# Kernel tuning notes

Measured on AMD Instinct MI355X. Metric: run time of the kernel, lower is better.

Reference implementation:

```python
import jax, jax.numpy as jnp
import numpy as np

B, T, E, H = 2, 2048, 1024, 16


def setup_inputs() -> dict:
    key = jax.random.key(0)
    ks = jax.random.split(key, 8)
    # VarianceScaling(1.0) ~ truncated normal with stddev ~ sqrt(1/fan_in)
    std = 1.0 / np.sqrt(E)
    x = jax.random.normal(ks[0], (B, T, E), dtype=jnp.float32)
    y = jax.random.normal(ks[1], (B, T, E), dtype=jnp.float32)
    # causal mask [1, 1, T, T]
    mask = jnp.tril(jnp.ones((T, T), dtype=jnp.float32))[None, None]
    Wq = jax.random.normal(ks[2], (E, E), dtype=jnp.float32) * std
    Wk = jax.random.normal(ks[3], (E, E), dtype=jnp.float32) * std
    Wv = jax.random.normal(ks[4], (E, E), dtype=jnp.float32) * std
    Wo = jax.random.normal(ks[5], (E, E), dtype=jnp.float32) * std
    bq = jnp.zeros((E,), jnp.float32)
    bk = jnp.zeros((E,), jnp.float32)
    bv = jnp.zeros((E,), jnp.float32)
    bo = jnp.zeros((E,), jnp.float32)
    return {"x": x, "y": y, "mask": mask, "Wq": Wq, "bq": bq,
            "Wk": Wk, "bk": bk, "Wv": Wv, "bv": bv, "Wo": Wo, "bo": bo,
            "num_heads": H}


def reference(x, y, mask, Wq, bq, Wk, bk, Wv, bv, Wo, bo, num_heads):
    Bx, Tq, Emb = x.shape
    Tkv = y.shape[1]
    d = Emb // num_heads
    q = (x @ Wq + bq).reshape(Bx, Tq, num_heads, d)
    k = (y @ Wk + bk).reshape(Bx, Tkv, num_heads, d)
    v = (y @ Wv + bv).reshape(Bx, Tkv, num_heads, d)
    scale = 1.0 / np.sqrt(d).astype(np.float32)
    att = scale * jnp.einsum('bthd,bThd->bhtT', q, k)  # [B,H,Tq,Tkv]
    att = att * mask - 1e10 * (1.0 - mask)
    att = jax.nn.softmax(att, axis=-1)
    out = jnp.einsum('bhtT,bThd->bthd', att, v).reshape(Bx, Tq, Emb)
    return out @ Wo + bo
```

## Files before the change

### kernel.cpp

```cpp
#include <hip/hip_runtime.h>
#include <stdint.h>

#define BB 2
#define TT 2048
#define EE 1024
#define HH 16
#define DD 64
#define MM (BB*TT)

typedef unsigned short u16;
typedef __attribute__((ext_vector_type(4))) float f32x4;
typedef __attribute__((ext_vector_type(8))) __bf16 bf16x8;
typedef __attribute__((ext_vector_type(8))) u16 u16x8;
typedef __attribute__((ext_vector_type(4))) u16 u16x4;

union FragU { u16x8 u; bf16x8 b; };
union BfU { __bf16 h; u16 u; };

__device__ __forceinline__ u16 f2bf(float f) {
  uint32_t u = __float_as_uint(f);
  u += 0x7fffu + ((u >> 16) & 1u);
  return (u16)(u >> 16);
}

__device__ __forceinline__ void gload16(const u16* __restrict__ g, u16* l) {
  __builtin_amdgcn_global_load_lds((const __attribute__((address_space(1))) void*)g,
                                   (__attribute__((address_space(3))) void*)l, 16, 0, 0);
}

__global__ __launch_bounds__(256) void prep(const float* __restrict__ x, const float* __restrict__ y,
                                            const float* __restrict__ Wq, const float* __restrict__ Wk,
                                            const float* __restrict__ Wv, const float* __restrict__ Wo,
                                            u16* __restrict__ xb, u16* __restrict__ yb,
                                            u16* __restrict__ Wqt, u16* __restrict__ Wkvt,
                                            u16* __restrict__ Wot) {
  __shared__ alignas(16) float tile[64][65];
  int bi = blockIdx.x, t = threadIdx.x;
  if (bi < 4096) {
    const float* src = (bi < 2048) ? x : y;
    u16* dst = (bi < 2048) ? xb : yb;
    int i = (bi & 2047) * 256 + t;
    const f32x4* s4 = (const f32x4*)src;
    f32x4 a = s4[2*i], b = s4[2*i+1];
    u16x8 o;
    o[0]=f2bf(a[0]); o[1]=f2bf(a[1]); o[2]=f2bf(a[2]); o[3]=f2bf(a[3]);
    o[4]=f2bf(b[0]); o[5]=f2bf(b[1]); o[6]=f2bf(b[2]); o[7]=f2bf(b[3]);
    ((u16x8*)dst)[i] = o;
    return;
  }
  int wi = bi - 4096;
  int z = wi >> 8;
  const float* W; u16* Tp;
  switch (z) {
    case 0: W = Wq; Tp = Wqt; break;
    case 1: W = Wk; Tp = Wkvt; break;
    case 2: W = Wv; Tp = Wkvt + (size_t)1024*EE; break;
    default: W = Wo; Tp = Wot; break;
  }
  int r8 = wi & 255;
  int n0 = (r8 & 15) * 64, k0 = (r8 >> 4) * 64;
#pragma unroll
  for (int i = 0; i < 16; ++i) {
    int idx = i*256 + t; int r = idx >> 6, c = idx & 63;
    tile[r][c] = W[(size_t)(k0 + r) * EE + n0 + c];
  }
  __syncthreads();
#pragma unroll
  for (int i = 0; i < 16; ++i) {
    int idx = i*256 + t; int rn = idx >> 6, ck = idx & 63;
    Tp[(size_t)(n0 + rn) * EE + k0 + ck] = f2bf(tile[ck][rn]);
  }
}

template <int BM, int EPI>
__device__ __forceinline__ void gemm_body(const u16* __restrict__ A, const u16* __restrict__ Bt,
                                          const float* __restrict__ bias, void* __restrict__ Cout,
                                          int N, int K, float oscale, int bm, int bn,
                                          u16 (*As)[64], u16 (*Bs)[64]) {
  constexpr int MI = (BM + 31) / 32;
  const int t = threadIdx.x;
  const int lane = t & 63, w = t >> 6;
  const int wr = w >> 1, wc = w & 1;
  const int g = lane >> 4, cl = lane & 15;

  f32x4 acc[MI][4] = {};

  const u16* Ag = A + (size_t)(bm * BM) * K;
  const u16* Bg = Bt + (size_t)(bn * 128) * K;

  const int rl = lane >> 3;
  const int sw = ((lane & 7) ^ rl) * 8;

  const int nk = K / 64;
  for (int kt = 0; kt < nk; ++kt) {
    const int k0 = kt * 64;
    __syncthreads();
    if (BM == 32) {
      gload16(Ag + (size_t)(w*8 + rl) * K + k0 + sw, &As[w*8][0]);
    } else {
#pragma unroll
      for (int j = 0; j < MI; ++j) {
        int ca = w * MI + j;
        gload16(Ag + (size_t)(ca*8 + rl) * K + k0 + sw, &As[ca*8][0]);
      }
    }
#pragma unroll
    for (int j = 0; j < 4; ++j) {
      int cb = w * 4 + j;
      gload16(Bg + (size_t)(cb*8 + rl) * K + k0 + sw, &Bs[cb*8][0]);
    }
    __syncthreads();
#pragma unroll
    for (int ks = 0; ks < 2; ++ks) {
      FragU af[MI], bfr[4];
#pragma unroll
      for (int mi = 0; mi < MI; ++mi) {
        int row = (BM == 32) ? (wr*16 + cl) : (wr*(BM/2) + mi*16 + cl);
        af[mi].u = *(const u16x8*)&As[row][((ks*4 + g) ^ (row & 7)) * 8];
      }
#pragma unroll
      for (int nj = 0; nj < 4; ++nj) {
        int row = wc*64 + nj*16 + cl;
        bfr[nj].u = *(const u16x8*)&Bs[row][((ks*4 + g) ^ (row & 7)) * 8];
      }
#pragma unroll
      for (int mi = 0; mi < MI; ++mi)
#pragma unroll
        for (int nj = 0; nj < 4; ++nj)
          acc[mi][nj] = __builtin_amdgcn_mfma_f32_16x16x32_bf16(af[mi].b, bfr[nj].b, acc[mi][nj], 0, 0, 0);
    }
  }

  const int cbase = bn*128 + wc*64 + cl;
  float bv[4];
#pragma unroll
  for (int nj = 0; nj < 4; ++nj) bv[nj] = bias[cbase + nj*16];
#pragma unroll
  for (int mi = 0; mi < MI; ++mi) {
    int row0 = (BM == 32) ? (bm*32 + wr*16 + (g << 2))
                          : (bm*BM + wr*(BM/2) + mi*16 + (g << 2));
    if (EPI == 2) {
      int bb = row0 >> 11;
      int tt = row0 & 2047;
      int tb64 = tt & ~63;
      int w6 = tt & 63;
      int p = ((w6 >> 5) << 5) | (((w6 >> 2) & 3) << 3) | (((w6 >> 4) & 1) << 2);
#pragma unroll
      for (int nj = 0; nj < 4; ++nj) {
        int cc = cbase + nj*16;
        int hh = cc >> 6, dd = cc & 63;
        u16x4 v;
#pragma unroll
        for (int i = 0; i < 4; ++i) v[i] = f2bf(acc[mi][nj][i] + bv[nj]);
        *(u16x4*)((u16*)Cout + ((size_t)((bb*HH + hh)*DD + dd))*2048 + tb64 + p) = v;
      }
    } else {
#pragma unroll
      for (int i = 0; i < 4; ++i) {
        if (EPI == 1) {
          float* Cp = (float*)Cout + (size_t)(row0 + i) * N + cbase;
#pragma unroll
          for (int nj = 0; nj < 4; ++nj)
            Cp[nj*16] = (acc[mi][nj][i] + bv[nj]) * oscale;
        } else {
          u16* Cp = (u16*)Cout + (size_t)(row0 + i) * N + cbase;
#pragma unroll
          for (int nj = 0; nj < 4; ++nj)
            Cp[nj*16] = f2bf((acc[mi][nj][i] + bv[nj]) * oscale);
        }
      }
    }
  }
}

__global__ __launch_bounds__(256) void gemm_qkv(const u16* __restrict__ xb, const u16* __restrict__ yb,
                                                const u16* __restrict__ Wqt, const u16* __restrict__ Wkvt,
                                                const float* __restrict__ bq, const float* __restrict__ bk,
                                                const float* __restrict__ bv,
                                                u16* __restrict__ Qb, u16* __restrict__ Kb,
                                                u16* __restrict__ Vtb, float c1) {
  __shared__ alignas(16) u16 As[64][64];
  __shared__ alignas(16) u16 Bs[128][64];
  const int i = blockIdx.x;
  const int l = (i & 7) * 192 + (i >> 3);
  const int bm = l / 24, bx = l % 24;
  if (bx < 8)
    gemm_body<64, 0>(xb, Wqt, bq, Qb, 1024, EE, c1, bm, bx, As, Bs);
  else if (bx < 16)
    gemm_body<64, 0>(yb, Wkvt, bk, Kb, 1024, EE, 1.0f, bm, bx - 8, As, Bs);
  else
    gemm_body<64, 2>(yb, Wkvt + (size_t)1024*EE, bv, Vtb, 1024, EE, 1.0f, bm, bx - 16, As, Bs);
}

__global__ __launch_bounds__(256) void gemm_o(const u16* __restrict__ Atb, const u16* __restrict__ Wot,
                                              const float* __restrict__ bo, float* __restrict__ out) {
  __shared__ alignas(16) u16 As[32][64];
  __shared__ alignas(16) u16 Bs[128][64];
  const int i = blockIdx.x;
  const int l = (i & 7) * 128 + (i >> 3);
  const int bm = l / 8, bn = l % 8;
  gemm_body<32, 1>(Atb, Wot, bo, out, 1024, EE, 1.0f, bm, bn, As, Bs);
}

__global__ __launch_bounds__(512, 4) void attn(const u16* __restrict__ Q, const u16* __restrict__ Kb,
                                               const u16* __restrict__ Vt, u16* __restrict__ O) {
  const int i0 = blockIdx.x;
  const int qp = i0 >> 5;
  const int bh = i0 & 31;
  const int b = bh >> 4, h = bh & 15;

  const int t = threadIdx.x, lane = t & 63, w = t >> 6;
  const int ws_ = w & 3;
  const int hi = w >> 2;
  const int g = lane >> 4, c = lane & 15;
  __shared__ alignas(16) u16 Ks[2][2][64][72];
  __shared__ alignas(16) u16 Vs[2][2][64][72];

  const u16* Kbase = Kb + (size_t)(b*TT) * 1024 + h*DD;
  const u16* Vtbase = Vt + (size_t)(b*HH + h) * DD * 2048;

  const int srow = t >> 3;
  const int scol = (t & 7) * 8;
  const int swc = scol ^ ((srow & 7) << 3);
  const int rxor = (c & 7) << 3;

  FragU onef;
#pragma unroll
  for (int e = 0; e < 8; ++e) onef.u[e] = 0x3F80;

  for (int pi = 0; pi < 2; ++pi) {
    const int qt = pi ? 31 - qp : qp;
    const int qw0 = qt * 64 + ws_ * 16;

    FragU qf[2];
    const u16* Qbase = Q + ((size_t)(b*TT) + qw0) * EE + h*DD;
#pragma unroll
    for (int ks = 0; ks < 2; ++ks)
      qf[ks].u = *(const u16x8*)(Qbase + (size_t)c * EE + ks*32 + g*8);

    f32x4 oacc[4] = {};
    f32x4 lacc = {};

    const int nkv = qt + 1;
    const int npair = (nkv + 1) >> 1;

    const u16* kp = Kbase + (size_t)srow * 1024 + scol;
    const u16* vp = Vtbase + (size_t)srow * 2048 + scol;

    u16x8 rk[2], rv[2];
    rk[0] = *(const u16x8*)kp;
    rv[0] = *(const u16x8*)vp;
    if (1 < nkv) {
      rk[1] = *(const u16x8*)(kp + 65536);
      rv[1] = *(const u16x8*)(vp + 64);
    }
    kp += 131072; vp += 128;

    __syncthreads();
    *(u16x8*)&Ks[0][0][srow][swc] = rk[0];
    *(u16x8*)&Vs[0][0][srow][swc] = rv[0];
    if (1 < nkv) {
      *(u16x8*)&Ks[0][1][srow][swc] = rk[1];
      *(u16x8*)&Vs[0][1][srow][swc] = rv[1];
    }
    __syncthreads();

    for (int jj = 0; jj < npair; ++jj) {
      const int d = jj & 1;
      const int j0 = 2*jj;
      if (jj + 1 < npair) {
        rk[0] = *(const u16x8*)kp;
        rv[0] = *(const u16x8*)vp;
        if (j0 + 3 < nkv) {
          rk[1] = *(const u16x8*)(kp + 65536);
          rv[1] = *(const u16x8*)(vp + 64);
        }
        kp += 131072; vp += 128;
      }

      const int j = j0 + hi;
      const int kv0 = j * 64;
      if (j < nkv && kv0 <= qw0 + 15) {
        f32x4 s[4] = {};
        __builtin_amdgcn_s_setprio(1);
#pragma unroll
        for (int ks = 0; ks < 2; ++ks) {
          const int kc = (ks*32 + g*8) ^ rxor;
          FragU kf[4];
#pragma unroll
          for (int nj = 0; nj < 4; ++nj)
            kf[nj].u = *(const u16x8*)&Ks[d][hi][nj*16 + c][kc];
#pragma unroll
          for (int nj = 0; nj < 4; ++nj)
            s[nj] = __builtin_amdgcn_mfma_f32_16x16x32_bf16(kf[nj].b, qf[ks].b, s[nj], 0, 0, 0);
        }
        __builtin_amdgcn_s_setprio(0);

        const bool full = (kv0 + 63 <= qw0);
        if (!full) {
          const int q = qw0 + c;
#pragma unroll
          for (int nj = 0; nj < 4; ++nj)
#pragma unroll
            for (int r = 0; r < 4; ++r)
              if (kv0 + nj*16 + 4*g + r > q) s[nj][r] = -1e30f;
        }

        FragU pa[2];
#pragma unroll
        for (int nj = 0; nj < 4; ++nj)
#pragma unroll
          for (int r = 0; r < 4; ++r) {
            float p = exp2f(s[nj][r]);
            BfU cv; cv.h = (__bf16)p;
            pa[nj >> 1].u[(nj & 1) * 4 + r] = cv.u;
          }

        __builtin_amdgcn_s_setprio(1);
#pragma unroll
        for (int ks = 0; ks < 2; ++ks) {
          const int vc = (ks*32 + g*8) ^ rxor;
#pragma unroll
          for (int dj = 0; dj < 4; ++dj) {
            FragU vf;
            vf.u = *(const u16x8*)&Vs[d][hi][dj*16 + c][vc];
            oacc[dj] = __builtin_amdgcn_mfma_f32_16x16x32_bf16(pa[ks].b, vf.b, oacc[dj], 0, 0, 0);
          }
          lacc = __builtin_amdgcn_mfma_f32_16x16x32_bf16(pa[ks].b, onef.b, lacc, 0, 0, 0);
        }
        __builtin_amdgcn_s_setprio(0);
      }

      if (jj + 1 < npair) {
        *(u16x8*)&Ks[d^1][0][srow][swc] = rk[0];
        *(u16x8*)&Vs[d^1][0][srow][swc] = rv[0];
        if (j0 + 3 < nkv) {
          *(u16x8*)&Ks[d^1][1][srow][swc] = rk[1];
          *(u16x8*)&Vs[d^1][1][srow][swc] = rv[1];
        }
        __syncthreads();
      }
    }

    __syncthreads();
    float* mO = (float*)&Ks[0][0][0][0];
    float* mL = (float*)&Vs[0][0][0][0];

    if (hi) {
#pragma unroll
      for (int i = 0; i < 4; ++i) {
        int row = 4*g + i;
#pragma unroll
        for (int dj = 0; dj < 4; ++dj)
          mO[((size_t)(ws_*16 + row))*66 + dj*16 + c] = oacc[dj][i];
      }
      if (c == 0) {
#pragma unroll
        for (int i = 0; i < 4; ++i) mL[ws_*16 + 4*g + i] = lacc[i];
      }
    }
    __syncthreads();
    if (!hi) {
      u16* Ob = O + ((size_t)(b*TT) + qw0) * EE + h*DD;
#pragma unroll
      for (int i = 0; i < 4; ++i) {
        int row = 4*g + i;
        float inv = 1.f / (lacc[i] + mL[ws_*16 + row]);
#pragma unroll
        for (int dj = 0; dj < 4; ++dj) {
          float o1 = mO[((size_t)(ws_*16 + row))*66 + dj*16 + c];
          Ob[(size_t)row * EE + dj*16 + c] = f2bf((oacc[dj][i] + o1) * inv);
        }
      }
    }
  }
}

extern "C" void kernel_launch(void* const* d_in, const int* in_sizes, int n_in,
                              void* d_out, int out_size, void* d_ws, size_t ws_size,
                              hipStream_t stream) {
  const float* x  = (const float*)d_in[0];
  const float* y  = (const float*)d_in[1];
  const float* Wq = (const float*)d_in[3];
  const float* bq = (const float*)d_in[4];
  const float* Wk = (const float*)d_in[5];
  const float* bk = (const float*)d_in[6];
  const float* Wv = (const float*)d_in[7];
  const float* bv = (const float*)d_in[8];
  const float* Wo = (const float*)d_in[9];
  const float* bo = (const float*)d_in[10];

  if (ws_size < (size_t)58720256) return;

  char* ws = (char*)d_ws;
  u16* Wqt  = (u16*)(ws + 0);
  u16* Wkvt = (u16*)(ws + 2097152);
  u16* Wot  = (u16*)(ws + 6291456);
  u16* Qb   = (u16*)(ws + 8388608);
  u16* Kb   = (u16*)(ws + 16777216);
  u16* Vtb  = (u16*)(ws + 25165824);
  u16* Atb  = (u16*)(ws + 33554432);
  u16* xb   = (u16*)(ws + 41943040);
  u16* yb   = (u16*)(ws + 50331648);

  const float c1 = 0.125f * 1.44269504088896340736f;

  prep<<<5120, 256, 0, stream>>>(x, y, Wq, Wk, Wv, Wo, xb, yb, Wqt, Wkvt, Wot);
  gemm_qkv<<<1536, 256, 0, stream>>>(xb, yb, Wqt, Wkvt, bq, bk, bv, Qb, Kb, Vtb, c1);
  attn<<<512, 512, 0, stream>>>(Qb, Kb, Vtb, Atb);
  gemm_o<<<1024, 256, 0, stream>>>(Atb, Wot, bo, (float*)d_out);
}
```

Measured before the change: 103.8 us.

## Fuse x/y bf16 conversion into QKV GEMM loads and drop attention LDS swizzle

Removes the separate fp32-to-bf16 conversion pass over x and y in the prep kernel. The QKV GEMM now reads fp32 activations directly, converts them in registers and stores swizzled bf16 tiles to LDS, which saves a round trip through global memory and shrinks the workspace. In exchange, each GEMM tile converts the activations again for every output column block, reads twice the bytes per A tile, and gives up the async global_load_lds path. The attention kernel's XOR swizzle on K/V shared tiles is also removed; with the 72-element padding this may change LDS bank conflicts.

```diff
diff --git a/kernel.cpp b/kernel.cpp
--- a/kernel.cpp
+++ b/kernel.cpp
@@ -23,32 +23,24 @@
   return (u16)(u >> 16);
 }
 
+__device__ __forceinline__ u16x8 cvt8(f32x4 a, f32x4 b) {
+  u16x8 o;
+  o[0]=f2bf(a[0]); o[1]=f2bf(a[1]); o[2]=f2bf(a[2]); o[3]=f2bf(a[3]);
+  o[4]=f2bf(b[0]); o[5]=f2bf(b[1]); o[6]=f2bf(b[2]); o[7]=f2bf(b[3]);
+  return o;
+}
+
 __device__ __forceinline__ void gload16(const u16* __restrict__ g, u16* l) {
   __builtin_amdgcn_global_load_lds((const __attribute__((address_space(1))) void*)g,
                                    (__attribute__((address_space(3))) void*)l, 16, 0, 0);
 }
 
-__global__ __launch_bounds__(256) void prep(const float* __restrict__ x, const float* __restrict__ y,
-                                            const float* __restrict__ Wq, const float* __restrict__ Wk,
+__global__ __launch_bounds__(256) void prep(const float* __restrict__ Wq, const float* __restrict__ Wk,
                                             const float* __restrict__ Wv, const float* __restrict__ Wo,
-                                            u16* __restrict__ xb, u16* __restrict__ yb,
                                             u16* __restrict__ Wqt, u16* __restrict__ Wkvt,
                                             u16* __restrict__ Wot) {
   __shared__ alignas(16) float tile[64][65];
-  int bi = blockIdx.x, t = threadIdx.x;
-  if (bi < 4096) {
-    const float* src = (bi < 2048) ? x : y;
-    u16* dst = (bi < 2048) ? xb : yb;
-    int i = (bi & 2047) * 256 + t;
-    const f32x4* s4 = (const f32x4*)src;
-    f32x4 a = s4[2*i], b = s4[2*i+1];
-    u16x8 o;
-    o[0]=f2bf(a[0]); o[1]=f2bf(a[1]); o[2]=f2bf(a[2]); o[3]=f2bf(a[3]);
-    o[4]=f2bf(b[0]); o[5]=f2bf(b[1]); o[6]=f2bf(b[2]); o[7]=f2bf(b[3]);
-    ((u16x8*)dst)[i] = o;
-    return;
-  }
-  int wi = bi - 4096;
+  int wi = blockIdx.x, t = threadIdx.x;
   int z = wi >> 8;
   const float* W; u16* Tp;
   switch (z) {
@@ -72,8 +64,8 @@
   }
 }
 
-template <int BM, int EPI>
-__device__ __forceinline__ void gemm_body(const u16* __restrict__ A, const u16* __restrict__ Bt,
+template <int BM, int EPI, bool AF32>
+__device__ __forceinline__ void gemm_body(const void* __restrict__ A, const u16* __restrict__ Bt,
                                           const float* __restrict__ bias, void* __restrict__ Cout,
                                           int N, int K, float oscale, int bm, int bn,
                                           u16 (*As)[64], u16 (*Bs)[64]) {
@@ -85,7 +77,8 @@
 
   f32x4 acc[MI][4] = {};
 
-  const u16* Ag = A + (size_t)(bm * BM) * K;
+  const u16* Ag16 = (const u16*)A + (size_t)(bm * BM) * K;
+  const float* Ag32 = (const float*)A + (size_t)(bm * BM) * K;
   const u16* Bg = Bt + (size_t)(bn * 128) * K;
 
   const int rl = lane >> 3;
@@ -95,13 +88,22 @@
   for (int kt = 0; kt < nk; ++kt) {
     const int k0 = kt * 64;
     __syncthreads();
-    if (BM == 32) {
-      gload16(Ag + (size_t)(w*8 + rl) * K + k0 + sw, &As[w*8][0]);
+    if (AF32) {
+      const int srow = t >> 3, scol = (t & 7) * 8;
+#pragma unroll
+      for (int r = 0; r < MI; ++r) {
+        int row = r*32 + srow;
+        const float* p = Ag32 + (size_t)row * K + k0 + scol;
+        u16x8 v = cvt8(*(const f32x4*)p, *(const f32x4*)(p + 4));
+        *(u16x8*)&As[row][scol ^ ((row & 7) << 3)] = v;
+      }
+    } else if (BM == 32) {
+      gload16(Ag16 + (size_t)(w*8 + rl) * K + k0 + sw, &As[w*8][0]);
     } else {
 #pragma unroll
       for (int j = 0; j < MI; ++j) {
         int ca = w * MI + j;
-        gload16(Ag + (size_t)(ca*8 + rl) * K + k0 + sw, &As[ca*8][0]);
+        gload16(Ag16 + (size_t)(ca*8 + rl) * K + k0 + sw, &As[ca*8][0]);
       }
     }
 #pragma unroll
@@ -173,7 +175,7 @@
   }
 }
 
-__global__ __launch_bounds__(256) void gemm_qkv(const u16* __restrict__ xb, const u16* __restrict__ yb,
+__global__ __launch_bounds__(256) void gemm_qkv(const float* __restrict__ x, const float* __restrict__ y,
                                                 const u16* __restrict__ Wqt, const u16* __restrict__ Wkvt,
                                                 const float* __restrict__ bq, const float* __restrict__ bk,
                                                 const float* __restrict__ bv,
@@ -185,11 +187,11 @@
   const int l = (i & 7) * 192 + (i >> 3);
   const int bm = l / 24, bx = l % 24;
   if (bx < 8)
-    gemm_body<64, 0>(xb, Wqt, bq, Qb, 1024, EE, c1, bm, bx, As, Bs);
+    gemm_body<64, 0, true>(x, Wqt, bq, Qb, 1024, EE, c1, bm, bx, As, Bs);
   else if (bx < 16)
-    gemm_body<64, 0>(yb, Wkvt, bk, Kb, 1024, EE, 1.0f, bm, bx - 8, As, Bs);
+    gemm_body<64, 0, true>(y, Wkvt, bk, Kb, 1024, EE, 1.0f, bm, bx - 8, As, Bs);
   else
-    gemm_body<64, 2>(yb, Wkvt + (size_t)1024*EE, bv, Vtb, 1024, EE, 1.0f, bm, bx - 16, As, Bs);
+    gemm_body<64, 2, true>(y, Wkvt + (size_t)1024*EE, bv, Vtb, 1024, EE, 1.0f, bm, bx - 16, As, Bs);
 }
 
 __global__ __launch_bounds__(256) void gemm_o(const u16* __restrict__ Atb, const u16* __restrict__ Wot,
@@ -199,7 +201,7 @@
   const int i = blockIdx.x;
   const int l = (i & 7) * 128 + (i >> 3);
   const int bm = l / 8, bn = l % 8;
-  gemm_body<32, 1>(Atb, Wot, bo, out, 1024, EE, 1.0f, bm, bn, As, Bs);
+  gemm_body<32, 1, false>(Atb, Wot, bo, out, 1024, EE, 1.0f, bm, bn, As, Bs);
 }
 
 __global__ __launch_bounds__(512, 4) void attn(const u16* __restrict__ Q, const u16* __restrict__ Kb,
@@ -221,8 +223,6 @@
 
   const int srow = t >> 3;
   const int scol = (t & 7) * 8;
-  const int swc = scol ^ ((srow & 7) << 3);
-  const int rxor = (c & 7) << 3;
 
   FragU onef;
 #pragma unroll
@@ -257,11 +257,11 @@
     kp += 131072; vp += 128;
 
     __syncthreads();
-    *(u16x8*)&Ks[0][0][srow][swc] = rk[0];
-    *(u16x8*)&Vs[0][0][srow][swc] = rv[0];
+    *(u16x8*)&Ks[0][0][srow][scol] = rk[0];
+    *(u16x8*)&Vs[0][0][srow][scol] = rv[0];
     if (1 < nkv) {
-      *(u16x8*)&Ks[0][1][srow][swc] = rk[1];
-      *(u16x8*)&Vs[0][1][srow][swc] = rv[1];
+      *(u16x8*)&Ks[0][1][srow][scol] = rk[1];
+      *(u16x8*)&Vs[0][1][srow][scol] = rv[1];
     }
     __syncthreads();
 
@@ -285,7 +285,7 @@
         __builtin_amdgcn_s_setprio(1);
 #pragma unroll
         for (int ks = 0; ks < 2; ++ks) {
-          const int kc = (ks*32 + g*8) ^ rxor;
+          const int kc = ks*32 + g*8;
           FragU kf[4];
 #pragma unroll
           for (int nj = 0; nj < 4; ++nj)
@@ -319,7 +319,7 @@
         __builtin_amdgcn_s_setprio(1);
 #pragma unroll
         for (int ks = 0; ks < 2; ++ks) {
-          const int vc = (ks*32 + g*8) ^ rxor;
+          const int vc = ks*32 + g*8;
 #pragma unroll
           for (int dj = 0; dj < 4; ++dj) {
             FragU vf;
@@ -332,11 +332,11 @@
       }
 
       if (jj + 1 < npair) {
-        *(u16x8*)&Ks[d^1][0][srow][swc] = rk[0];
-        *(u16x8*)&Vs[d^1][0][srow][swc] = rv[0];
+        *(u16x8*)&Ks[d^1][0][srow][scol] = rk[0];
+        *(u16x8*)&Vs[d^1][0][srow][scol] = rv[0];
         if (j0 + 3 < nkv) {
-          *(u16x8*)&Ks[d^1][1][srow][swc] = rk[1];
-          *(u16x8*)&Vs[d^1][1][srow][swc] = rv[1];
+          *(u16x8*)&Ks[d^1][1][srow][scol] = rk[1];
+          *(u16x8*)&Vs[d^1][1][srow][scol] = rv[1];
         }
         __syncthreads();
       }
@@ -390,7 +390,7 @@
   const float* Wo = (const float*)d_in[9];
   const float* bo = (const float*)d_in[10];
 
-  if (ws_size < (size_t)58720256) return;
+  if (ws_size < (size_t)41943040) return;
 
   char* ws = (char*)d_ws;
   u16* Wqt  = (u16*)(ws + 0);
@@ -400,13 +400,11 @@
   u16* Kb   = (u16*)(ws + 16777216);
   u16* Vtb  = (u16*)(ws + 25165824);
   u16* Atb  = (u16*)(ws + 33554432);
-  u16* xb   = (u16*)(ws + 41943040);
-  u16* yb   = (u16*)(ws + 50331648);
 
   const float c1 = 0.125f * 1.44269504088896340736f;
 
-  prep<<<5120, 256, 0, stream>>>(x, y, Wq, Wk, Wv, Wo, xb, yb, Wqt, Wkvt, Wot);
-  gemm_qkv<<<1536, 256, 0, stream>>>(xb, yb, Wqt, Wkvt, bq, bk, bv, Qb, Kb, Vtb, c1);
+  prep<<<1024, 256, 0, stream>>>(Wq, Wk, Wv, Wo, Wqt, Wkvt, Wot);
+  gemm_qkv<<<1536, 256, 0, stream>>>(x, y, Wqt, Wkvt, bq, bk, bv, Qb, Kb, Vtb, c1);
   attn<<<512, 512, 0, stream>>>(Qb, Kb, Vtb, Atb);
   gemm_o<<<1024, 256, 0, stream>>>(Atb, Wot, bo, (float*)d_out);
 }
```

Result: slower. 106.1 us (+2.3%).
